# Kernel tuning notes

Hardware: AMD Instinct MI355X
Metric: run time of the kernel (lower is better)

## Reference

```python
import jax, jax.numpy as jnp
import numpy as np

IN_FEATURES = [32, 32]
OUT_FEATURES = [64, 64]
RANKS = [16, 16, 16, 16]


def _make_cores(key):
    dims = IN_FEATURES + OUT_FEATURES
    ranks = RANKS
    # init scale as in the torch module
    var = 2 ** (1.0 / len(dims)) / np.prod(np.power(np.array(ranks) + np.array(IN_FEATURES + IN_FEATURES), 1.0 / len(dims)))
    ub = float(np.sqrt(3.0 * var))
    ranks_ext = [ranks[-1]] + list(ranks)
    cores = []
    for i in range(len(dims)):
        key, k = jax.random.split(key)
        cores.append(jax.random.uniform(k, (ranks_ext[i], dims[i], ranks_ext[i + 1]), jnp.float32, -ub, ub))
    return cores, key


def setup_inputs() -> dict:
    key = jax.random.key(0)
    cores, key = _make_cores(key)
    key, kx, kb = jax.random.split(key, 3)
    x = jax.random.normal(kx, (8192, int(np.prod(IN_FEATURES))), jnp.float32)
    bias = jax.random.normal(kb, (int(np.prod(OUT_FEATURES)),), jnp.float32)
    return {"x": x, "core0": cores[0], "core1": cores[1], "core2": cores[2], "core3": cores[3], "bias": bias}


def reference(x, core0, core1, core2, core3, bias):
    # Tensor-ring contraction to build the dense weight, then linear.
    # core shapes: (16,32,16), (16,32,16), (16,64,16), (16,64,16)
    w = jnp.tensordot(core0, core1, axes=([2], [0]))        # (r, i0, i1, r)
    w = jnp.tensordot(w, core2, axes=([3], [0]))            # (r, i0, i1, o0, r)
    # last core: contract w's trailing rank with core axis 0 AND w's leading
    # rank with core's trailing rank (closes the ring) -> (i0, i1, o0, o1)
    w = jnp.tensordot(w, core3, axes=([4, 0], [0, 2]))
    d_out = int(np.prod(OUT_FEATURES))
    w = w.reshape(d_out, -1)                                # (4096, 1024)
    return x @ w.T + bias
```

## Files before the change

kernel.cpp:

```cpp
#include <hip/hip_runtime.h>
#include <hip/hip_bf16.h>
#include <stdint.h>

typedef unsigned short ushort_t;
typedef __attribute__((ext_vector_type(8))) short short8;
typedef __attribute__((ext_vector_type(4))) float floatx4;

__device__ __forceinline__ ushort_t f2bf(float f) {
    union { float f; unsigned u; } v; v.f = f;
    unsigned r = v.u + 0x7fffu + ((v.u >> 16) & 1u);
    return (ushort_t)(r >> 16);
}

__device__ __forceinline__ void async16(ushort_t* lds, const ushort_t* g) {
    __builtin_amdgcn_global_load_lds(
        (const __attribute__((address_space(1))) unsigned int*)g,
        (__attribute__((address_space(3))) unsigned int*)lds, 16, 0, 0);
}

__global__ __launch_bounds__(256) void prep_all(const float* __restrict__ x,
                                                const float* __restrict__ c0,
                                                const float* __restrict__ c1,
                                                const float* __restrict__ c2,
                                                const float* __restrict__ c3,
                                                ushort_t* __restrict__ Xb,
                                                ushort_t* __restrict__ A2b,
                                                ushort_t* __restrict__ B2t) {
    const int b = blockIdx.x, t = threadIdx.x;
    if (b < 8192) {
        int i = b * 256 + t;
        float4 v = ((const float4*)x)[i];
        ushort4 r;
        r.x = f2bf(v.x); r.y = f2bf(v.y); r.z = f2bf(v.z); r.w = f2bf(v.w);
        ((ushort4*)Xb)[i] = r;
    } else if (b < 9216) {
        int id = (b - 8192) * 256 + t;
        int k = id & 255, ii = id >> 8;
        int r0 = k >> 4, r2 = k & 15;
        int i0 = ii >> 5, i1 = ii & 31;
        const float* p0 = c0 + (r0 * 32 + i0) * 16;
        const float* p1 = c1 + i1 * 16 + r2;
        float s = 0.f;
#pragma unroll
        for (int r1 = 0; r1 < 16; r1++) s += p0[r1] * p1[r1 * 512];
        A2b[id] = f2bf(s);
    } else {
        int id = (b - 9216) * 256 + t;
        int k = id & 255, oo = id >> 8;
        int r0 = k >> 4, r2 = k & 15;
        int o0 = oo >> 6, o1 = oo & 63;
        const float* p2 = c2 + (r2 * 64 + o0) * 16;
        const float* p3 = c3 + o1 * 16 + r0;
        float s = 0.f;
#pragma unroll
        for (int r3 = 0; r3 < 16; r3++) s += p2[r3] * p3[r3 * 1024];
        B2t[id] = f2bf(s);
    }
}

__global__ __launch_bounds__(256) void build_w_mfma(const ushort_t* __restrict__ A2b,
                                                    const ushort_t* __restrict__ B2t,
                                                    ushort_t* __restrict__ W) {
    __shared__ ushort_t As[128 * 32];
    __shared__ ushort_t Bs[128 * 32];
    const int t = threadIdx.x;
    const int row0 = blockIdx.x * 128;
    const int col0 = blockIdx.y * 128;
    const int w = t >> 6, l = t & 63;
    const int wm = w >> 1, wn = w & 1;
    const int quad = l >> 4, ln = l & 15;

    floatx4 acc[4][4] = {};

    const ushort_t* aSrc = A2b + (size_t)(row0 + (t >> 2)) * 256 + (t & 3) * 8;
    const ushort_t* bSrc = B2t + (size_t)(col0 + (t >> 2)) * 256 + (t & 3) * 8;

    for (int kk = 0; kk < 256; kk += 32) {
        async16(&As[t * 8],        aSrc + kk);
        async16(&As[2048 + t * 8], aSrc + 64 * 256 + kk);
        async16(&Bs[t * 8],        bSrc + kk);
        async16(&Bs[2048 + t * 8], bSrc + 64 * 256 + kk);
        __syncthreads();

        short8 a[4], b[4];
#pragma unroll
        for (int ti = 0; ti < 4; ti++)
            a[ti] = *(const short8*)&As[(wm * 64 + ti * 16 + ln) * 32 + quad * 8];
#pragma unroll
        for (int tj = 0; tj < 4; tj++)
            b[tj] = *(const short8*)&Bs[(wn * 64 + tj * 16 + ln) * 32 + quad * 8];
#pragma unroll
        for (int ti = 0; ti < 4; ti++)
#pragma unroll
            for (int tj = 0; tj < 4; tj++)
                acc[ti][tj] = __builtin_amdgcn_mfma_f32_16x16x32_bf16(
                    a[ti], b[tj], acc[ti][tj], 0, 0, 0);
        __syncthreads();
    }

#pragma unroll
    for (int tj = 0; tj < 4; tj++) {
        const int n = col0 + wn * 64 + tj * 16 + ln;
#pragma unroll
        for (int ti = 0; ti < 4; ti++) {
            const int m = row0 + wm * 64 + ti * 16 + quad * 4;
#pragma unroll
            for (int r = 0; r < 4; r++)
                W[(size_t)(m + r) * 4096 + n] = f2bf(acc[ti][tj][r]);
        }
    }
}

__global__ __launch_bounds__(256) void gemm_bt_bias(const ushort_t* __restrict__ Xb,
                                                    const ushort_t* __restrict__ Wb,
                                                    const float* __restrict__ bias,
                                                    float* __restrict__ out) {
    __shared__ ushort_t As[128 * 32];
    __shared__ ushort_t Bs[128 * 32];
    const int t = threadIdx.x;
    const int row0 = blockIdx.x * 128;
    const int col0 = blockIdx.y * 128;
    const int w = t >> 6, l = t & 63;
    const int wm = w >> 1, wn = w & 1;
    const int quad = l >> 4, ln = l & 15;

    floatx4 acc[4][4] = {};

    const ushort_t* aSrc = Xb + (size_t)(row0 + (t >> 2)) * 1024 + (t & 3) * 8;
    const ushort_t* bSrc = Wb + (size_t)(col0 + (t >> 2)) * 1024 + (t & 3) * 8;

    for (int kk = 0; kk < 1024; kk += 32) {
        async16(&As[t * 8],        aSrc + kk);
        async16(&As[2048 + t * 8], aSrc + 64 * 1024 + kk);
        async16(&Bs[t * 8],        bSrc + kk);
        async16(&Bs[2048 + t * 8], bSrc + 64 * 1024 + kk);
        __syncthreads();

        short8 a[4], b[4];
#pragma unroll
        for (int ti = 0; ti < 4; ti++)
            a[ti] = *(const short8*)&As[(wm * 64 + ti * 16 + ln) * 32 + quad * 8];
#pragma unroll
        for (int tj = 0; tj < 4; tj++)
            b[tj] = *(const short8*)&Bs[(wn * 64 + tj * 16 + ln) * 32 + quad * 8];
#pragma unroll
        for (int ti = 0; ti < 4; ti++)
#pragma unroll
            for (int tj = 0; tj < 4; tj++)
                acc[ti][tj] = __builtin_amdgcn_mfma_f32_16x16x32_bf16(
                    a[ti], b[tj], acc[ti][tj], 0, 0, 0);
        __syncthreads();
    }

#pragma unroll
    for (int tj = 0; tj < 4; tj++) {
        const int n = col0 + wn * 64 + tj * 16 + ln;
        const float bv = bias[n];
#pragma unroll
        for (int ti = 0; ti < 4; ti++) {
            const int m = row0 + wm * 64 + ti * 16 + quad * 4;
            float* o = out + (size_t)m * 4096 + n;
#pragma unroll
            for (int r = 0; r < 4; r++)
                o[(size_t)r * 4096] = acc[ti][tj][r] + bv;
        }
    }
}

extern "C" void kernel_launch(void* const* d_in, const int* in_sizes, int n_in,
                              void* d_out, int out_size, void* d_ws, size_t ws_size,
                              hipStream_t stream) {
    const float* x    = (const float*)d_in[0];
    const float* c0   = (const float*)d_in[1];
    const float* c1   = (const float*)d_in[2];
    const float* c2   = (const float*)d_in[3];
    const float* c3   = (const float*)d_in[4];
    const float* bias = (const float*)d_in[5];
    float* out = (float*)d_out;

    char* ws = (char*)d_ws;
    ushort_t* Xb  = (ushort_t*)ws;
    ushort_t* Wb  = (ushort_t*)(ws + (16u << 20));
    ushort_t* A2b = (ushort_t*)(ws + (24u << 20));
    ushort_t* B2t = (ushort_t*)(ws + (25u << 20));

    hipLaunchKernelGGL(prep_all, dim3(13312), dim3(256), 0, stream,
                       x, c0, c1, c2, c3, Xb, A2b, B2t);
    hipLaunchKernelGGL(build_w_mfma, dim3(8, 32), dim3(256), 0, stream, A2b, B2t, Wb);
    hipLaunchKernelGGL(gemm_bt_bias, dim3(64, 32), dim3(256), 0, stream, Xb, Wb, bias, out);
}
```

Measured before the change: 255.1 us.

## Reorder tensor-ring contraction to avoid building dense weight

Replaces materializing the dense 4096x1024 weight followed by one large GEMM with a two-stage factorized contraction: x is multiplied by a packed core-pair factor into an intermediate Z, then Z is contracted block-wise with the other core-pair factor plus bias. The x fp32-to-bf16 conversion is fused into the first GEMM's tile loads. This cuts total matrix FLOPs and removes the W build and the separate conversion pass, at the cost of writing and rereading a bf16 intermediate and a less regular second GEMM with small per-block K.

```diff
diff --git a/kernel.cpp b/kernel.cpp
--- a/kernel.cpp
+++ b/kernel.cpp
@@ -12,55 +12,58 @@
     return (ushort_t)(r >> 16);
 }
 
+__device__ __forceinline__ short8 pack8(float4 a, float4 b) {
+    short8 r;
+    r[0] = (short)f2bf(a.x); r[1] = (short)f2bf(a.y);
+    r[2] = (short)f2bf(a.z); r[3] = (short)f2bf(a.w);
+    r[4] = (short)f2bf(b.x); r[5] = (short)f2bf(b.y);
+    r[6] = (short)f2bf(b.z); r[7] = (short)f2bf(b.w);
+    return r;
+}
+
 __device__ __forceinline__ void async16(ushort_t* lds, const ushort_t* g) {
     __builtin_amdgcn_global_load_lds(
         (const __attribute__((address_space(1))) unsigned int*)g,
         (__attribute__((address_space(3))) unsigned int*)lds, 16, 0, 0);
 }
 
-__global__ __launch_bounds__(256) void prep_all(const float* __restrict__ x,
-                                                const float* __restrict__ c0,
-                                                const float* __restrict__ c1,
-                                                const float* __restrict__ c2,
-                                                const float* __restrict__ c3,
-                                                ushort_t* __restrict__ Xb,
-                                                ushort_t* __restrict__ A2b,
-                                                ushort_t* __restrict__ B2t) {
-    const int b = blockIdx.x, t = threadIdx.x;
-    if (b < 8192) {
-        int i = b * 256 + t;
-        float4 v = ((const float4*)x)[i];
-        ushort4 r;
-        r.x = f2bf(v.x); r.y = f2bf(v.y); r.z = f2bf(v.z); r.w = f2bf(v.w);
-        ((ushort4*)Xb)[i] = r;
-    } else if (b < 9216) {
-        int id = (b - 8192) * 256 + t;
-        int k = id & 255, ii = id >> 8;
+
+__global__ __launch_bounds__(256) void prep(const float* __restrict__ c0,
+                                            const float* __restrict__ c1,
+                                            const float* __restrict__ c2,
+                                            const float* __restrict__ c3,
+                                            ushort_t* __restrict__ V,
+                                            ushort_t* __restrict__ A2b) {
+    const int blk = blockIdx.x, t = threadIdx.x;
+    if (blk < 4096) {
+        int id = blk * 256 + t;
+        int c = id & 1023, kp = id >> 10;
+        int b = kp >> 8, k = kp & 255;
         int r0 = k >> 4, r2 = k & 15;
-        int i0 = ii >> 5, i1 = ii & 31;
+        int o0 = b * 16 + (c >> 6), o1 = c & 63;
+        const float* p2 = c2 + (r2 * 64 + o0) * 16;
+        const float* p3 = c3 + o1 * 16 + r0;
+        float s = 0.f;
+#pragma unroll
+        for (int r3 = 0; r3 < 16; r3++) s += p2[r3] * p3[r3 * 1024];
+        V[id] = f2bf(s);
+    } else {
+        int id = (blk - 4096) * 256 + t;
+        int k = id & 255, a = id >> 8;
+        int r0 = k >> 4, r2 = k & 15;
+        int i0 = a >> 5, i1 = a & 31;
         const float* p0 = c0 + (r0 * 32 + i0) * 16;
         const float* p1 = c1 + i1 * 16 + r2;
         float s = 0.f;
 #pragma unroll
         for (int r1 = 0; r1 < 16; r1++) s += p0[r1] * p1[r1 * 512];
         A2b[id] = f2bf(s);
-    } else {
-        int id = (b - 9216) * 256 + t;
-        int k = id & 255, oo = id >> 8;
-        int r0 = k >> 4, r2 = k & 15;
-        int o0 = oo >> 6, o1 = oo & 63;
-        const float* p2 = c2 + (r2 * 64 + o0) * 16;
-        const float* p3 = c3 + o1 * 16 + r0;
-        float s = 0.f;
-#pragma unroll
-        for (int r3 = 0; r3 < 16; r3++) s += p2[r3] * p3[r3 * 1024];
-        B2t[id] = f2bf(s);
-    }
-}
-
-__global__ __launch_bounds__(256) void build_w_mfma(const ushort_t* __restrict__ A2b,
-                                                    const ushort_t* __restrict__ B2t,
-                                                    ushort_t* __restrict__ W) {
+    }
+}
+
+__global__ __launch_bounds__(256) void gemm_z(const float* __restrict__ x,
+                                              const ushort_t* __restrict__ V,
+                                              ushort_t* __restrict__ Z) {
     __shared__ ushort_t As[128 * 32];
     __shared__ ushort_t Bs[128 * 32];
     const int t = threadIdx.x;
@@ -72,14 +75,18 @@
 
     floatx4 acc[4][4] = {};
 
-    const ushort_t* aSrc = A2b + (size_t)(row0 + (t >> 2)) * 256 + (t & 3) * 8;
-    const ushort_t* bSrc = B2t + (size_t)(col0 + (t >> 2)) * 256 + (t & 3) * 8;
-
-    for (int kk = 0; kk < 256; kk += 32) {
-        async16(&As[t * 8],        aSrc + kk);
-        async16(&As[2048 + t * 8], aSrc + 64 * 256 + kk);
+    const float*    aSrc = x + (size_t)(row0 + (t >> 2)) * 1024 + (t & 3) * 8;
+    const ushort_t* bSrc = V + (size_t)(col0 + (t >> 2)) * 1024 + (t & 3) * 8;
+
+    for (int kk = 0; kk < 1024; kk += 32) {
         async16(&Bs[t * 8],        bSrc + kk);
-        async16(&Bs[2048 + t * 8], bSrc + 64 * 256 + kk);
+        async16(&Bs[2048 + t * 8], bSrc + 64 * 1024 + kk);
+        float4 f0 = *(const float4*)(aSrc + kk);
+        float4 f1 = *(const float4*)(aSrc + kk + 4);
+        float4 f2 = *(const float4*)(aSrc + 64 * 1024 + kk);
+        float4 f3 = *(const float4*)(aSrc + 64 * 1024 + kk + 4);
+        *(short8*)&As[t * 8]        = pack8(f0, f1);
+        *(short8*)&As[2048 + t * 8] = pack8(f2, f3);
         __syncthreads();
 
         short8 a[4], b[4];
@@ -106,63 +113,73 @@
             const int m = row0 + wm * 64 + ti * 16 + quad * 4;
 #pragma unroll
             for (int r = 0; r < 4; r++)
-                W[(size_t)(m + r) * 4096 + n] = f2bf(acc[ti][tj][r]);
+                Z[(size_t)(m + r) * 1024 + n] = f2bf(acc[ti][tj][r]);
         }
     }
 }
 
-__global__ __launch_bounds__(256) void gemm_bt_bias(const ushort_t* __restrict__ Xb,
-                                                    const ushort_t* __restrict__ Wb,
-                                                    const float* __restrict__ bias,
-                                                    float* __restrict__ out) {
-    __shared__ ushort_t As[128 * 32];
-    __shared__ ushort_t Bs[128 * 32];
+__global__ __launch_bounds__(256) void gemm_out(const ushort_t* __restrict__ Z,
+                                                const ushort_t* __restrict__ A2b,
+                                                const float* __restrict__ bias,
+                                                float* __restrict__ out) {
+    __shared__ ushort_t Zs[2 * 128 * 32];
+    __shared__ ushort_t A2s[32 * 264];
     const int t = threadIdx.x;
     const int row0 = blockIdx.x * 128;
     const int col0 = blockIdx.y * 128;
+    const int a0 = col0 >> 2;
     const int w = t >> 6, l = t & 63;
     const int wm = w >> 1, wn = w & 1;
     const int quad = l >> 4, ln = l & 15;
 
     floatx4 acc[4][4] = {};
 
-    const ushort_t* aSrc = Xb + (size_t)(row0 + (t >> 2)) * 1024 + (t & 3) * 8;
-    const ushort_t* bSrc = Wb + (size_t)(col0 + (t >> 2)) * 1024 + (t & 3) * 8;
-
-    for (int kk = 0; kk < 1024; kk += 32) {
-        async16(&As[t * 8],        aSrc + kk);
-        async16(&As[2048 + t * 8], aSrc + 64 * 1024 + kk);
-        async16(&Bs[t * 8],        bSrc + kk);
-        async16(&Bs[2048 + t * 8], bSrc + 64 * 1024 + kk);
-        __syncthreads();
-
-        short8 a[4], b[4];
-#pragma unroll
-        for (int ti = 0; ti < 4; ti++)
-            a[ti] = *(const short8*)&As[(wm * 64 + ti * 16 + ln) * 32 + quad * 8];
-#pragma unroll
-        for (int tj = 0; tj < 4; tj++)
-            b[tj] = *(const short8*)&Bs[(wn * 64 + tj * 16 + ln) * 32 + quad * 8];
-#pragma unroll
-        for (int ti = 0; ti < 4; ti++)
-#pragma unroll
-            for (int tj = 0; tj < 4; tj++)
-                acc[ti][tj] = __builtin_amdgcn_mfma_f32_16x16x32_bf16(
-                    a[ti], b[tj], acc[ti][tj], 0, 0, 0);
-        __syncthreads();
-    }
-
-#pragma unroll
-    for (int tj = 0; tj < 4; tj++) {
-        const int n = col0 + wn * 64 + tj * 16 + ln;
-        const float bv = bias[n];
-#pragma unroll
-        for (int ti = 0; ti < 4; ti++) {
-            const int m = row0 + wm * 64 + ti * 16 + quad * 4;
-            float* o = out + (size_t)m * 4096 + n;
-#pragma unroll
-            for (int r = 0; r < 4; r++)
-                o[(size_t)r * 4096] = acc[ti][tj][r] + bv;
+#pragma unroll
+    for (int q = 0; q < 4; q++) {
+        int g = q * 2048 + t * 8;
+        int r = g >> 8, cidx = g & 255;
+        short8 v = *(const short8*)(A2b + (size_t)(a0 + r) * 256 + cidx);
+        *(short8*)&A2s[r * 264 + cidx] = v;
+    }
+
+    const ushort_t* zSrc = Z + (size_t)(row0 + (t >> 2)) * 1024 + (t & 3) * 8;
+
+#pragma unroll
+    for (int b = 0; b < 4; b++) {
+        for (int kk = 0; kk < 256; kk += 64) {
+            const ushort_t* src = zSrc + b * 256 + kk;
+            async16(&Zs[t * 8],        src);
+            async16(&Zs[2048 + t * 8], src + 64 * 1024);
+            async16(&Zs[4096 + t * 8], src + 32);
+            async16(&Zs[6144 + t * 8], src + 64 * 1024 + 32);
+            __syncthreads();
+#pragma unroll
+            for (int half = 0; half < 2; half++) {
+                short8 bb = *(const short8*)&A2s[(wn * 16 + ln) * 264 + kk + half * 32 + quad * 8];
+#pragma unroll
+                for (int ti = 0; ti < 4; ti++) {
+                    short8 av = *(const short8*)&Zs[half * 4096 + (wm * 64 + ti * 16 + ln) * 32 + quad * 8];
+                    acc[ti][b] = __builtin_amdgcn_mfma_f32_16x16x32_bf16(
+                        av, bb, acc[ti][b], 0, 0, 0);
+                }
+            }
+            __syncthreads();
+        }
+    }
+
+    const int aIdx = a0 + wn * 16 + ln;
+    const float4 bv = *(const float4*)(bias + aIdx * 4);
+#pragma unroll
+    for (int ti = 0; ti < 4; ti++) {
+#pragma unroll
+        for (int r = 0; r < 4; r++) {
+            const int s = row0 + wm * 64 + ti * 16 + quad * 4 + r;
+            float4 o;
+            o.x = acc[ti][0][r] + bv.x;
+            o.y = acc[ti][1][r] + bv.y;
+            o.z = acc[ti][2][r] + bv.z;
+            o.w = acc[ti][3][r] + bv.w;
+            *(float4*)(out + (size_t)s * 4096 + aIdx * 4) = o;
         }
     }
 }
@@ -179,13 +196,11 @@
     float* out = (float*)d_out;
 
     char* ws = (char*)d_ws;
-    ushort_t* Xb  = (ushort_t*)ws;
-    ushort_t* Wb  = (ushort_t*)(ws + (16u << 20));
-    ushort_t* A2b = (ushort_t*)(ws + (24u << 20));
-    ushort_t* B2t = (ushort_t*)(ws + (25u << 20));
-
-    hipLaunchKernelGGL(prep_all, dim3(13312), dim3(256), 0, stream,
-                       x, c0, c1, c2, c3, Xb, A2b, B2t);
-    hipLaunchKernelGGL(build_w_mfma, dim3(8, 32), dim3(256), 0, stream, A2b, B2t, Wb);
-    hipLaunchKernelGGL(gemm_bt_bias, dim3(64, 32), dim3(256), 0, stream, Xb, Wb, bias, out);
-}
+    ushort_t* V   = (ushort_t*)ws;
+    ushort_t* A2b = (ushort_t*)(ws + (2u << 20));
+    ushort_t* Zb  = (ushort_t*)(ws + (4u << 20));
+
+    hipLaunchKernelGGL(prep, dim3(5120), dim3(256), 0, stream, c0, c1, c2, c3, V, A2b);
+    hipLaunchKernelGGL(gemm_z, dim3(64, 8), dim3(256), 0, stream, x, V, Zb);
+    hipLaunchKernelGGL(gemm_out, dim3(64, 32), dim3(256), 0, stream, Zb, A2b, bias, out);
+}
```

After: 258.2 us. About the same (+1.2%).

## Factor tensor-ring weight into two smaller GEMMs instead of materializing dense W

Applied to the files above, without the earlier changes.

Stops building the dense 4096x1024 weight and multiplying by it. The first GEMM contracts the input against the (c2,c3) factor to get an 8192x1024 bf16 intermediate Z. A second batched GEMM then contracts Z against the (c0,c1) factor over the rank pair and adds the bias. This cuts total MAC work roughly in half. In exchange it adds an extra bf16 rounding of Z, and the output stores become strided by four columns, which may reduce store coalescing.

```diff
diff --git a/kernel.cpp b/kernel.cpp
--- a/kernel.cpp
+++ b/kernel.cpp
@@ -18,148 +18,151 @@
         (__attribute__((address_space(3))) unsigned int*)lds, 16, 0, 0);
 }
 
+
 __global__ __launch_bounds__(256) void prep_all(const float* __restrict__ x,
                                                 const float* __restrict__ c0,
                                                 const float* __restrict__ c1,
                                                 const float* __restrict__ c2,
                                                 const float* __restrict__ c3,
                                                 ushort_t* __restrict__ Xb,
-                                                ushort_t* __restrict__ A2b,
-                                                ushort_t* __restrict__ B2t) {
-    const int b = blockIdx.x, t = threadIdx.x;
-    if (b < 8192) {
-        int i = b * 256 + t;
+                                                ushort_t* __restrict__ V,
+                                                ushort_t* __restrict__ A2b) {
+    const int blk = blockIdx.x, t = threadIdx.x;
+    if (blk < 8192) {
+        int i = blk * 256 + t;
         float4 v = ((const float4*)x)[i];
         ushort4 r;
         r.x = f2bf(v.x); r.y = f2bf(v.y); r.z = f2bf(v.z); r.w = f2bf(v.w);
         ((ushort4*)Xb)[i] = r;
-    } else if (b < 9216) {
-        int id = (b - 8192) * 256 + t;
-        int k = id & 255, ii = id >> 8;
+    } else if (blk < 12288) {
+        int id = (blk - 8192) * 256 + t;
+        int c = id & 1023, kp = id >> 10;
+        int b = kp >> 8, k = kp & 255;
         int r0 = k >> 4, r2 = k & 15;
-        int i0 = ii >> 5, i1 = ii & 31;
+        int o0 = b * 16 + (c >> 6), o1 = c & 63;
+        const float* p2 = c2 + (r2 * 64 + o0) * 16;
+        const float* p3 = c3 + o1 * 16 + r0;
+        float s = 0.f;
+#pragma unroll
+        for (int r3 = 0; r3 < 16; r3++) s += p2[r3] * p3[r3 * 1024];
+        V[id] = f2bf(s);
+    } else {
+        int id = (blk - 12288) * 256 + t;
+        int k = id & 255, a = id >> 8;
+        int r0 = k >> 4, r2 = k & 15;
+        int i0 = a >> 5, i1 = a & 31;
         const float* p0 = c0 + (r0 * 32 + i0) * 16;
         const float* p1 = c1 + i1 * 16 + r2;
         float s = 0.f;
 #pragma unroll
         for (int r1 = 0; r1 < 16; r1++) s += p0[r1] * p1[r1 * 512];
         A2b[id] = f2bf(s);
-    } else {
-        int id = (b - 9216) * 256 + t;
-        int k = id & 255, oo = id >> 8;
-        int r0 = k >> 4, r2 = k & 15;
-        int o0 = oo >> 6, o1 = oo & 63;
-        const float* p2 = c2 + (r2 * 64 + o0) * 16;
-        const float* p3 = c3 + o1 * 16 + r0;
-        float s = 0.f;
-#pragma unroll
-        for (int r3 = 0; r3 < 16; r3++) s += p2[r3] * p3[r3 * 1024];
-        B2t[id] = f2bf(s);
     }
 }
 
-__global__ __launch_bounds__(256) void build_w_mfma(const ushort_t* __restrict__ A2b,
-                                                    const ushort_t* __restrict__ B2t,
-                                                    ushort_t* __restrict__ W) {
+__global__ __launch_bounds__(256) void gemm_z(const ushort_t* __restrict__ Xb,
+                                              const ushort_t* __restrict__ V,
+                                              ushort_t* __restrict__ Z) {
+    __shared__ ushort_t As[128 * 32];
+    __shared__ ushort_t Bs[64 * 32];
+    const int t = threadIdx.x;
+    const int row0 = blockIdx.x * 128;
+    const int col0 = blockIdx.y * 64;
+    const int w = t >> 6, l = t & 63;
+    const int wm = w >> 1, wn = w & 1;
+    const int quad = l >> 4, ln = l & 15;
+
+    floatx4 acc[4][2] = {};
+
+    const ushort_t* aSrc = Xb + (size_t)(row0 + (t >> 2)) * 1024 + (t & 3) * 8;
+    const ushort_t* bSrc = V  + (size_t)(col0 + (t >> 2)) * 1024 + (t & 3) * 8;
+
+    for (int kk = 0; kk < 1024; kk += 32) {
+        async16(&As[t * 8],        aSrc + kk);
+        async16(&As[2048 + t * 8], aSrc + 64 * 1024 + kk);
+        async16(&Bs[t * 8],        bSrc + kk);
+        __syncthreads();
+
+        short8 a[4], b[2];
+#pragma unroll
+        for (int ti = 0; ti < 4; ti++)
+            a[ti] = *(const short8*)&As[(wm * 64 + ti * 16 + ln) * 32 + quad * 8];
+#pragma unroll
+        for (int tj = 0; tj < 2; tj++)
+            b[tj] = *(const short8*)&Bs[(wn * 32 + tj * 16 + ln) * 32 + quad * 8];
+#pragma unroll
+        for (int ti = 0; ti < 4; ti++)
+#pragma unroll
+            for (int tj = 0; tj < 2; tj++)
+                acc[ti][tj] = __builtin_amdgcn_mfma_f32_16x16x32_bf16(
+                    a[ti], b[tj], acc[ti][tj], 0, 0, 0);
+        __syncthreads();
+    }
+
+#pragma unroll
+    for (int tj = 0; tj < 2; tj++) {
+        const int n = col0 + wn * 32 + tj * 16 + ln;
+#pragma unroll
+        for (int ti = 0; ti < 4; ti++) {
+            const int m = row0 + wm * 64 + ti * 16 + quad * 4;
+#pragma unroll
+            for (int r = 0; r < 4; r++)
+                Z[(size_t)(m + r) * 1024 + n] = f2bf(acc[ti][tj][r]);
+        }
+    }
+}
+
+__global__ __launch_bounds__(256) void gemm_out(const ushort_t* __restrict__ Z,
+                                                const ushort_t* __restrict__ A2b,
+                                                const float* __restrict__ bias,
+                                                float* __restrict__ out) {
     __shared__ ushort_t As[128 * 32];
     __shared__ ushort_t Bs[128 * 32];
     const int t = threadIdx.x;
     const int row0 = blockIdx.x * 128;
-    const int col0 = blockIdx.y * 128;
+    const int a0 = (blockIdx.y >> 2) * 128;
+    const int b  = blockIdx.y & 3;
     const int w = t >> 6, l = t & 63;
     const int wm = w >> 1, wn = w & 1;
     const int quad = l >> 4, ln = l & 15;
 
     floatx4 acc[4][4] = {};
 
-    const ushort_t* aSrc = A2b + (size_t)(row0 + (t >> 2)) * 256 + (t & 3) * 8;
-    const ushort_t* bSrc = B2t + (size_t)(col0 + (t >> 2)) * 256 + (t & 3) * 8;
+    const ushort_t* aSrc = Z   + (size_t)(row0 + (t >> 2)) * 1024 + b * 256 + (t & 3) * 8;
+    const ushort_t* bSrc = A2b + (size_t)(a0   + (t >> 2)) * 256  + (t & 3) * 8;
 
     for (int kk = 0; kk < 256; kk += 32) {
         async16(&As[t * 8],        aSrc + kk);
-        async16(&As[2048 + t * 8], aSrc + 64 * 256 + kk);
+        async16(&As[2048 + t * 8], aSrc + 64 * 1024 + kk);
         async16(&Bs[t * 8],        bSrc + kk);
         async16(&Bs[2048 + t * 8], bSrc + 64 * 256 + kk);
         __syncthreads();
 
-        short8 a[4], b[4];
+        short8 a[4], bb[4];
 #pragma unroll
         for (int ti = 0; ti < 4; ti++)
             a[ti] = *(const short8*)&As[(wm * 64 + ti * 16 + ln) * 32 + quad * 8];
 #pragma unroll
         for (int tj = 0; tj < 4; tj++)
-            b[tj] = *(const short8*)&Bs[(wn * 64 + tj * 16 + ln) * 32 + quad * 8];
+            bb[tj] = *(const short8*)&Bs[(wn * 64 + tj * 16 + ln) * 32 + quad * 8];
 #pragma unroll
         for (int ti = 0; ti < 4; ti++)
 #pragma unroll
             for (int tj = 0; tj < 4; tj++)
                 acc[ti][tj] = __builtin_amdgcn_mfma_f32_16x16x32_bf16(
-                    a[ti], b[tj], acc[ti][tj], 0, 0, 0);
+                    a[ti], bb[tj], acc[ti][tj], 0, 0, 0);
         __syncthreads();
     }
 
 #pragma unroll
     for (int tj = 0; tj < 4; tj++) {
-        const int n = col0 + wn * 64 + tj * 16 + ln;
+        const int aIdx = a0 + wn * 64 + tj * 16 + ln;
+        const int j = aIdx * 4 + b;
+        const float bv = bias[j];
 #pragma unroll
         for (int ti = 0; ti < 4; ti++) {
             const int m = row0 + wm * 64 + ti * 16 + quad * 4;
-#pragma unroll
-            for (int r = 0; r < 4; r++)
-                W[(size_t)(m + r) * 4096 + n] = f2bf(acc[ti][tj][r]);
-        }
-    }
-}
-
-__global__ __launch_bounds__(256) void gemm_bt_bias(const ushort_t* __restrict__ Xb,
-                                                    const ushort_t* __restrict__ Wb,
-                                                    const float* __restrict__ bias,
-                                                    float* __restrict__ out) {
-    __shared__ ushort_t As[128 * 32];
-    __shared__ ushort_t Bs[128 * 32];
-    const int t = threadIdx.x;
-    const int row0 = blockIdx.x * 128;
-    const int col0 = blockIdx.y * 128;
-    const int w = t >> 6, l = t & 63;
-    const int wm = w >> 1, wn = w & 1;
-    const int quad = l >> 4, ln = l & 15;
-
-    floatx4 acc[4][4] = {};
-
-    const ushort_t* aSrc = Xb + (size_t)(row0 + (t >> 2)) * 1024 + (t & 3) * 8;
-    const ushort_t* bSrc = Wb + (size_t)(col0 + (t >> 2)) * 1024 + (t & 3) * 8;
-
-    for (int kk = 0; kk < 1024; kk += 32) {
-        async16(&As[t * 8],        aSrc + kk);
-        async16(&As[2048 + t * 8], aSrc + 64 * 1024 + kk);
-        async16(&Bs[t * 8],        bSrc + kk);
-        async16(&Bs[2048 + t * 8], bSrc + 64 * 1024 + kk);
-        __syncthreads();
-
-        short8 a[4], b[4];
-#pragma unroll
-        for (int ti = 0; ti < 4; ti++)
-            a[ti] = *(const short8*)&As[(wm * 64 + ti * 16 + ln) * 32 + quad * 8];
-#pragma unroll
-        for (int tj = 0; tj < 4; tj++)
-            b[tj] = *(const short8*)&Bs[(wn * 64 + tj * 16 + ln) * 32 + quad * 8];
-#pragma unroll
-        for (int ti = 0; ti < 4; ti++)
-#pragma unroll
-            for (int tj = 0; tj < 4; tj++)
-                acc[ti][tj] = __builtin_amdgcn_mfma_f32_16x16x32_bf16(
-                    a[ti], b[tj], acc[ti][tj], 0, 0, 0);
-        __syncthreads();
-    }
-
-#pragma unroll
-    for (int tj = 0; tj < 4; tj++) {
-        const int n = col0 + wn * 64 + tj * 16 + ln;
-        const float bv = bias[n];
-#pragma unroll
-        for (int ti = 0; ti < 4; ti++) {
-            const int m = row0 + wm * 64 + ti * 16 + quad * 4;
-            float* o = out + (size_t)m * 4096 + n;
+            float* o = out + (size_t)m * 4096 + j;
 #pragma unroll
             for (int r = 0; r < 4; r++)
                 o[(size_t)r * 4096] = acc[ti][tj][r] + bv;
@@ -180,12 +183,12 @@
 
     char* ws = (char*)d_ws;
     ushort_t* Xb  = (ushort_t*)ws;
-    ushort_t* Wb  = (ushort_t*)(ws + (16u << 20));
-    ushort_t* A2b = (ushort_t*)(ws + (24u << 20));
-    ushort_t* B2t = (ushort_t*)(ws + (25u << 20));
+    ushort_t* V   = (ushort_t*)(ws + (16u << 20));
+    ushort_t* A2b = (ushort_t*)(ws + (18u << 20));
+    ushort_t* Zb  = (ushort_t*)(ws + (20u << 20));
 
     hipLaunchKernelGGL(prep_all, dim3(13312), dim3(256), 0, stream,
-                       x, c0, c1, c2, c3, Xb, A2b, B2t);
-    hipLaunchKernelGGL(build_w_mfma, dim3(8, 32), dim3(256), 0, stream, A2b, B2t, Wb);
-    hipLaunchKernelGGL(gemm_bt_bias, dim3(64, 32), dim3(256), 0, stream, Xb, Wb, bias, out);
+                       x, c0, c1, c2, c3, Xb, V, A2b);
+    hipLaunchKernelGGL(gemm_z,   dim3(64, 16), dim3(256), 0, stream, Xb, V, Zb);
+    hipLaunchKernelGGL(gemm_out, dim3(64, 32), dim3(256), 0, stream, Zb, A2b, bias, out);
 }
```

Result: slower. 287.3 us (+12.6%).
